# Kernel tuning notes

Measured on AMD Instinct MI355X. Metric: run time of the kernel, lower is better.

The kernel has to match this reference:

```python
import jax, jax.numpy as jnp
import numpy as np

RADIUS = 0.1
WEIGHT = 0.2
MATMUL_NORM = False


def setup_inputs() -> dict:
    key = jax.random.key(0)
    k1, k2, k3, k4, k5 = jax.random.split(key, 5)
    S, B, Ck, Cv, H, W = 8, 2, 64, 64, 64, 64
    return {
        "memory_keys": jax.random.normal(k1, (S, B, Ck, H, W), jnp.float32),
        "memory_values": jax.random.normal(k2, (S, B, Cv, H, W), jnp.float32),
        "query_query": jax.random.normal(k3, (B, Ck, H, W), jnp.float32),
        "disparity": jax.random.normal(k4, (B, 1, H, W), jnp.float32),
        "sequence_index": jax.random.randint(k5, (B, S, 2), 0, 10, jnp.int32),
    }


def reference(memory_keys, memory_values, query_query, disparity, sequence_index):
    S, B, Ck, H, W = memory_keys.shape
    Cv = memory_values.shape[2]
    HW, SHW = H * W, S * H * W

    # keys: [B, Ck, S*H*W]; queries: [B, H*W, Ck]
    keys = jnp.transpose(memory_keys, (1, 2, 0, 3, 4)).reshape(B, Ck, SHW)
    q = jnp.transpose(query_query.reshape(B, Ck, HW), (0, 2, 1))

    # disparity-based additive mask, vectorized over frames
    weight = WEIGHT / S / H / W
    idx = sequence_index.astype(jnp.float32)
    dist = jnp.sqrt((idx[:, :, 1] - 5.0) ** 2 + (idx[:, :, 0] - 5.0) ** 2)  # [B, S]
    total_disp = dist[:, :, None, None] * disparity  # [B, S, H, W] (disparity [B,1,H,W])
    mask = jnp.where(jnp.abs(total_disp) > RADIUS, weight, 0.0).reshape(B, 1, SHW)

    attn = jnp.einsum("bnc,bcm->bnm", q, keys)  # [B, HW, SHW]
    if MATMUL_NORM:
        attn = attn * (Ck ** -0.5)
    attn = jax.nn.softmax(attn, axis=-1) + mask

    vals = jnp.transpose(memory_values, (1, 0, 3, 4, 2)).reshape(B, SHW, Cv)
    out = jnp.einsum("bnm,bmv->bnv", attn, vals)  # [B, HW, Cv]
    return jnp.transpose(out, (0, 2, 1)).reshape(B, Cv, H, W)
```

## Files before the change

### kernel.cpp

```cpp
#include <hip/hip_runtime.h>
#include <hip/hip_bf16.h>
#include <stdint.h>

#define NS   8
#define NB   2
#define CK   64
#define CV   64
#define HWN  4096
#define SHW  32768
#define RADIUS_ 0.1f
#define MASK_W  6.103515625e-6f

#define TM    32
#define NW    8
#define QS_STR 68
#define P_STR  40
#define SBIAS 24.0f
#define LOG2E 1.4426950408889634f
#define SBIAS2 34.624680981135326f
#define KS    4

#define KT_ELEMS (NS * NB * CK * HWN)
#define KT_BYTES ((size_t)KT_ELEMS * 2)
#define VB_BYTES ((size_t)KT_ELEMS * 2)
#define MASKP_OFF (KT_BYTES + VB_BYTES)
#define WS_NEED  (MASKP_OFF + 4096)
#define ONUM_OFF (MASKP_OFF + 4096)
#define ONUM_BYTES ((size_t)KS * NB * HWN * CV * 4)
#define ODEN_OFF (ONUM_OFF + ONUM_BYTES)
#define ODEN_BYTES ((size_t)KS * NB * HWN * 4)
#define WS2      (ODEN_OFF + ODEN_BYTES)

typedef __bf16    bf16x8 __attribute__((ext_vector_type(8)));
typedef _Float16  f16x8  __attribute__((ext_vector_type(8)));
typedef float     f32x4  __attribute__((ext_vector_type(4)));
typedef unsigned short u16x8 __attribute__((ext_vector_type(8)));
typedef uint32_t  u32x2 __attribute__((ext_vector_type(2)));
typedef uint32_t  u32x4 __attribute__((ext_vector_type(4)));

__device__ __forceinline__ unsigned short f2bfu(float x) {
  __hip_bfloat16 h = __float2bfloat16(x);
  return __builtin_bit_cast(unsigned short, h);
}
__device__ __forceinline__ bf16x8 ld_bf8_lds(const unsigned short* p) {
  u16x8 u = *(const u16x8*)p;
  return __builtin_bit_cast(bf16x8, u);
}
__device__ __forceinline__ void load_lds16(const void* g, void* l) {
  __builtin_amdgcn_global_load_lds(
      (const __attribute__((address_space(1))) unsigned int*)g,
      (__attribute__((address_space(3))) unsigned int*)l, 16, 0, 0);
}


__global__ __launch_bounds__(512) void prep_all(
    const float* __restrict__ keys, const float* __restrict__ vals,
    const float* __restrict__ disp, const int* __restrict__ seq,
    _Float16* __restrict__ kT, unsigned short* __restrict__ vbf,
    float* __restrict__ maskpart)
{
  const int t = threadIdx.x;
  const int blk = blockIdx.x;
  if (blk < 512) {
    __shared__ _Float16 lds[128 * 64];
    const int chunk = blk & 31;
    const int s     = (blk >> 5) & 7;
    const int b     = blk >> 8;
    const int hw0   = chunk * 128;
    const int c_st  = t >> 3;
    const int msub  = (t & 7) * 8;
    const int cchunk = c_st >> 3;
    const int clow   = c_st & 7;

    const float* krow = keys + ((size_t)((s * NB + b) * CK + c_st)) * HWN + hw0;
    #pragma unroll
    for (int r = 0; r < 2; ++r) {
      const int m0 = msub + r * 64;
      f32x4 k0 = *(const f32x4*)(krow + m0);
      f32x4 k1 = *(const f32x4*)(krow + m0 + 4);
      const int swz = (cchunk ^ ((m0 >> 3) & 7)) * 8 + clow;
      #pragma unroll
      for (int j = 0; j < 4; ++j) {
        lds[(m0 + j)     * 64 + swz] = (_Float16)k0[j];
        lds[(m0 + 4 + j) * 64 + swz] = (_Float16)k1[j];
      }
    }
    __syncthreads();

    _Float16* kout = kT + ((size_t)(b * SHW + s * HWN + hw0)) * CK;
    const int mm = t >> 3;
    const int cg = t & 7;
    #pragma unroll
    for (int r2 = 0; r2 < 2; ++r2) {
      const int m   = mm + r2 * 64;
      const int swz = cg ^ ((m >> 3) & 7);
      u16x8 v = *(const u16x8*)&lds[m * 64 + swz * 8];
      *(u16x8*)(kout + (size_t)m * CK + cg * 8) = v;
    }
  } else {
    const int r = blk - 512;
    const int s = r >> 7;
    const int b = (r >> 6) & 1;
    const int c = r & 63;
    float j0 = (float)seq[(b * NS + s) * 2 + 0];
    float j1 = (float)seq[(b * NS + s) * 2 + 1];
    const float dist = sqrtf((j1 - 5.f) * (j1 - 5.f) + (j0 - 5.f) * (j0 - 5.f));

    const size_t i = (size_t)r * HWN + t * 8;
    const int hw = t * 8;
    f32x4 a  = *(const f32x4*)(vals + i);
    f32x4 bb = *(const f32x4*)(vals + i + 4);
    f32x4 d0 = *(const f32x4*)(disp + (size_t)b * HWN + hw);
    f32x4 d1 = *(const f32x4*)(disp + (size_t)b * HWN + hw + 4);
    u16x8 o;
    float acc = 0.f;
    #pragma unroll
    for (int j = 0; j < 4; ++j) {
      o[j]     = f2bfu(a[j]);
      o[4 + j] = f2bfu(bb[j]);
      if (fabsf(dist * d0[j]) > RADIUS_) acc += a[j];
      if (fabsf(dist * d1[j]) > RADIUS_) acc += bb[j];
    }
    {
      const int m  = t & 3;
      const int pa = ((2 * m) & 3) * 2 + (m >> 1);
      const int pb = ((2 * m + 1) & 3) * 2 + (m >> 1);
      unsigned short* rowp = vbf + (size_t)r * HWN + (t >> 2) * 32;
      u32x4 wv = __builtin_bit_cast(u32x4, o);
      *(u32x2*)(rowp + pa * 4) = (u32x2){wv.x, wv.y};
      *(u32x2*)(rowp + pb * 4) = (u32x2){wv.z, wv.w};
    }

    #pragma unroll
    for (int m2 = 32; m2 >= 1; m2 >>= 1) acc += __shfl_xor(acc, m2);
    __shared__ float red[8];
    if ((t & 63) == 0) red[t >> 6] = acc;
    __syncthreads();
    if (t == 0) {
      float s8 = 0.f;
      #pragma unroll
      for (int j = 0; j < 8; ++j) s8 += red[j];
      maskpart[(b * CV + c) * NS + s] = MASK_W * s8;
    }
  }
}

struct __align__(16) Smem6 {
  union {
    struct {
      _Float16       kbuf[2][128 * 64];
      unsigned short vbuf[2][64 * 128];
    } main;
    struct {
      float obuf[4][32][64];
      float dbuf[4][32];
    } epi;
    float qs[64 * QS_STR];
  };
};

__global__ __launch_bounds__(512, 4) void attn_v6(
    const _Float16* __restrict__ kT,
    const unsigned short* __restrict__ vbf,
    const float* __restrict__ query,
    float* __restrict__ onum,
    float* __restrict__ odenom)
{
  __shared__ Smem6 sm;
  const int t    = threadIdx.x;
  const int w    = t >> 6;
  const int lane = t & 63;
  const int quad = lane >> 4;
  const int l15  = lane & 15;
  const int kq   = w & 3;
  const int rg   = w >> 2;
  const int bidx = blockIdx.x;
  const int xcd  = bidx & 7;
  const int b    = xcd & 1;
  const int ks   = xcd >> 1;
  const int tile = bidx >> 3;
  const int n0   = tile * 64;

  {
    const int qc   = t >> 3;
    const int noff = (t & 7) * 8;
    const int slot = qc ^ ((t & 7) << 2);
    const float* qp = query + (size_t)(b * CK + qc) * HWN + n0 + noff;
    f32x4 q0 = *(const f32x4*)(qp);
    f32x4 q1 = *(const f32x4*)(qp + 4);
    #pragma unroll
    for (int j = 0; j < 4; ++j) {
      sm.qs[(noff + j)     * QS_STR + slot] = q0[j];
      sm.qs[(noff + 4 + j) * QS_STR + slot] = q1[j];
    }
  }
  __syncthreads();
  f16x8 qf[2][2];
  #pragma unroll
  for (int f = 0; f < 2; ++f) {
    const int n  = rg * 32 + f * 16 + l15;
    const int sw = ((n >> 3) & 7) << 2;
    const float* base = &sm.qs[n * QS_STR];
    #pragma unroll
    for (int h = 0; h < 2; ++h) {
      const int c0 = (h * 32 + quad * 8) ^ sw;
      f32x4 a  = *(const f32x4*)(base + c0);
      f32x4 bb = *(const f32x4*)(base + (c0 ^ 4));
      f16x8 q;
      #pragma unroll
      for (int j = 0; j < 4; ++j) {
        q[j]     = (_Float16)(a[j]  * LOG2E);
        q[4 + j] = (_Float16)(bb[j] * LOG2E);
      }
      qf[f][h] = q;
    }
  }
  __syncthreads();

  f32x4 Of[2][4];
  f32x4 Ol[2];
  #pragma unroll
  for (int f = 0; f < 2; ++f) {
    #pragma unroll
    for (int cf = 0; cf < 4; ++cf) Of[f][cf] = (f32x4){0.f, 0.f, 0.f, 0.f};
    Ol[f] = (f32x4){0.f, 0.f, 0.f, 0.f};
  }
  bf16x8 vones;
  #pragma unroll
  for (int i = 0; i < 8; ++i)
    vones[i] = __builtin_bit_cast(__bf16, (unsigned short)0x3F80);

  uint32_t ksrc_off[2];
  int      kldsoff[2];
  uint32_t vsrc_off[2];
  int      vldsoff[2];
  #pragma unroll
  for (int j = 0; j < 2; ++j) {
    const int inst = w * 2 + j;
    const int kl   = inst * 8 + (lane >> 3);
    const int cqs  = lane & 7;
    ksrc_off[j] = (uint32_t)(kl * 128 + ((cqs ^ (kl & 7)) * 16));
    kldsoff[j]  = inst * 1024;
    const int cv  = inst * 4 + (lane >> 4);
    const int chs = (lane & 15) ^ (cv & 7);
    vsrc_off[j] = (uint32_t)(cv * HWN + chs * 8);
    vldsoff[j]  = inst * 1024;
  }
  const char* kgbase = (const char*)(kT + (size_t)b * SHW * CK);
  const int   kbase0 = ks * (SHW / KS);

  {
    const char* kg = kgbase + (size_t)kbase0 * 128;
    load_lds16(kg + ksrc_off[0], (char*)sm.main.kbuf[0] + kldsoff[0]);
    load_lds16(kg + ksrc_off[1], (char*)sm.main.kbuf[0] + kldsoff[1]);
    const int sfrm0 = kbase0 >> 12;
    const unsigned short* vg =
        vbf + (size_t)((sfrm0 * NB + b) * CV) * HWN + (kbase0 & 4095);
    load_lds16(vg + vsrc_off[0], (char*)sm.main.vbuf[0] + vldsoff[0]);
    load_lds16(vg + vsrc_off[1], (char*)sm.main.vbuf[0] + vldsoff[1]);
  }

  for (int it = 0; it < 64; ++it) {
    const int cur  = it & 1;
    const int key0 = kbase0 + it * 128;

    __syncthreads();

    if (it < 63) {
      const int keyn = key0 + 128;
      const char* kg = kgbase + (size_t)keyn * 128;
      load_lds16(kg + ksrc_off[0], (char*)sm.main.kbuf[cur ^ 1] + kldsoff[0]);
      load_lds16(kg + ksrc_off[1], (char*)sm.main.kbuf[cur ^ 1] + kldsoff[1]);
      const int sfrmn = keyn >> 12;
      const unsigned short* vg =
          vbf + (size_t)((sfrmn * NB + b) * CV) * HWN + (keyn & 4095);
      load_lds16(vg + vsrc_off[0], (char*)sm.main.vbuf[cur ^ 1] + vldsoff[0]);
      load_lds16(vg + vsrc_off[1], (char*)sm.main.vbuf[cur ^ 1] + vldsoff[1]);
    }

    f16x8 kf[2][2];
    #pragma unroll
    for (int g = 0; g < 2; ++g) {
      const int kl  = kq * 32 + g * 16 + l15;
      const int swz = kl & 7;
      const _Float16* kb = &sm.main.kbuf[cur][kl * 64];
      #pragma unroll
      for (int h = 0; h < 2; ++h) {
        const int slot = (h * 4 + quad) ^ swz;
        kf[g][h] = *(const f16x8*)(kb + slot * 8);
      }
    }

    bf16x8 vf[4];
    {
      const int ch = kq * 4 + quad;
      #pragma unroll
      for (int cf = 0; cf < 4; ++cf) {
        const int cv  = cf * 16 + l15;
        const int swz = cv & 7;
        vf[cf] = ld_bf8_lds(&sm.main.vbuf[cur][cv * 128 + ((ch ^ swz) << 3)]);
      }
    }

    f32x4 sf[2][2];
    #pragma unroll
    for (int g = 0; g < 2; ++g)
      #pragma unroll
      for (int f = 0; f < 2; ++f) {
        f32x4 acc = (f32x4){-SBIAS2, -SBIAS2, -SBIAS2, -SBIAS2};
        acc = __builtin_amdgcn_mfma_f32_16x16x32_f16(kf[g][0], qf[f][0], acc, 0, 0, 0);
        acc = __builtin_amdgcn_mfma_f32_16x16x32_f16(kf[g][1], qf[f][1], acc, 0, 0, 0);
        sf[g][f] = acc;
      }

    #pragma unroll
    for (int f = 0; f < 2; ++f) {
      uint32_t pk[2][2];
      #pragma unroll
      for (int g = 0; g < 2; ++g) {
        float e0 = __builtin_amdgcn_exp2f(sf[g][f][0]);
        float e1 = __builtin_amdgcn_exp2f(sf[g][f][1]);
        float e2 = __builtin_amdgcn_exp2f(sf[g][f][2]);
        float e3 = __builtin_amdgcn_exp2f(sf[g][f][3]);
        pk[g][0] = __builtin_amdgcn_perm(__builtin_bit_cast(uint32_t, e1),
                                         __builtin_bit_cast(uint32_t, e0),
                                         0x07060302u);
        pk[g][1] = __builtin_amdgcn_perm(__builtin_bit_cast(uint32_t, e3),
                                         __builtin_bit_cast(uint32_t, e2),
                                         0x07060302u);
      }
      bf16x8 pf = __builtin_bit_cast(bf16x8,
          (u32x4){pk[0][0], pk[0][1], pk[1][0], pk[1][1]});

      #pragma unroll
      for (int cf = 0; cf < 4; ++cf)
        Of[f][cf] = __builtin_amdgcn_mfma_f32_16x16x32_bf16(pf, vf[cf], Of[f][cf], 0, 0, 0);
      Ol[f] = __builtin_amdgcn_mfma_f32_16x16x32_bf16(pf, vones, Ol[f], 0, 0, 0);
    }
  }

  __syncthreads();

  #pragma unroll
  for (int phase = 0; phase < 2; ++phase) {
    if (rg == phase) {
      #pragma unroll
      for (int f = 0; f < 2; ++f)
        #pragma unroll
        for (int r = 0; r < 4; ++r) {
          const int row = f * 16 + quad * 4 + r;
          if (l15 == 0) sm.epi.dbuf[kq][row] = Ol[f][r];
          #pragma unroll
          for (int cf = 0; cf < 4; ++cf)
            sm.epi.obuf[kq][row][cf * 16 + l15] = Of[f][cf][r];
        }
    }
    __syncthreads();
    {
      const int row = t >> 4;
      const int v4  = (t & 15) * 4;
      f32x4 acc = *(const f32x4*)&sm.epi.obuf[0][row][v4];
      #pragma unroll
      for (int q = 1; q < 4; ++q)
        acc += *(const f32x4*)&sm.epi.obuf[q][row][v4];
      *(f32x4*)&onum[((size_t)(ks * NB + b) * HWN + n0 + phase * 32 + row) * CV + v4] = acc;
      if (t < 32) {
        float d = sm.epi.dbuf[0][t] + sm.epi.dbuf[1][t] +
                  sm.epi.dbuf[2][t] + sm.epi.dbuf[3][t];
        odenom[(size_t)(ks * NB + b) * HWN + n0 + phase * 32 + t] = d;
      }
    }
    __syncthreads();
  }
}

__global__ __launch_bounds__(256) void finalize_k(
    const float* __restrict__ onum, const float* __restrict__ odenom,
    const float* __restrict__ maskpart, float* __restrict__ out)
{
  __shared__ float tile[64][68];
  __shared__ float dinv[64];
  __shared__ float ml[64];
  const int t   = threadIdx.x;
  const int b   = blockIdx.x >> 6;
  const int hw0 = (blockIdx.x & 63) * 64;

  #pragma unroll
  for (int pass = 0; pass < 4; ++pass) {
    const int row = pass * 16 + (t >> 4);
    const int v4  = (t & 15) * 4;
    f32x4 acc = (f32x4){0.f, 0.f, 0.f, 0.f};
    #pragma unroll
    for (int ks = 0; ks < KS; ++ks)
      acc += *(const f32x4*)&onum[((size_t)(ks * NB + b) * HWN + hw0 + row) * CV + v4];
    *(f32x4*)&tile[row][v4] = acc;
  }
  if (t < 64) {
    float d = 0.f;
    #pragma unroll
    for (int ks = 0; ks < KS; ++ks)
      d += odenom[(size_t)(ks * NB + b) * HWN + hw0 + t];
    dinv[t] = 1.f / fmaxf(d, 1e-30f);
  }
  if (t >= 64 && t < 128) {
    float m = 0.f;
    #pragma unroll
    for (int s = 0; s < NS; ++s) m += maskpart[(b * CV + (t - 64)) * NS + s];
    ml[t - 64] = m;
  }
  __syncthreads();

  #pragma unroll
  for (int pass = 0; pass < 4; ++pass) {
    const int v   = pass * 16 + (t >> 4);
    const int hw4 = (t & 15) * 4;
    f32x4 o;
    #pragma unroll
    for (int j = 0; j < 4; ++j)
      o[j] = tile[hw4 + j][v] * dinv[hw4 + j] + ml[v];
    *(f32x4*)&out[((size_t)(b * CV + v)) * HWN + hw0 + hw4] = o;
  }
}

struct __align__(16) SmemF {
  union {
    float qs[TM * QS_STR];
    unsigned short p[NW][2][16 * P_STR];
    struct {
      float obuf[NW][TM][CV];
      float lbuf[NW][TM];
    } epi;
  };
};

__global__ __launch_bounds__(512) void attn_fast(
    const _Float16* __restrict__ kT, const unsigned short* __restrict__ vbf,
    const float* __restrict__ query, const float* __restrict__ maskpart,
    float* __restrict__ out)
{
  __shared__ SmemF sm;
  const int t    = threadIdx.x;
  const int w    = t >> 6;
  const int lane = t & 63;
  const int quad = lane >> 4;
  const int l15  = lane & 15;
  const int bidx = blockIdx.x;
  const int b    = bidx & 1;
  const int n0   = ((bidx >> 1) & 127) * TM;

  if (t < 256) {
    const int qc   = t >> 2;
    const int noff = (t & 3) * 8;
    const int slot = qc ^ ((t & 3) << 2);
    const float* qp = query + (size_t)(b * CK + qc) * HWN + n0 + noff;
    f32x4 q0 = *(const f32x4*)(qp);
    f32x4 q1 = *(const f32x4*)(qp + 4);
    #pragma unroll
    for (int j = 0; j < 4; ++j) {
      sm.qs[(noff + j)     * QS_STR + slot] = q0[j];
      sm.qs[(noff + 4 + j) * QS_STR + slot] = q1[j];
    }
  }
  __syncthreads();
  f16x8 qf[2][2];
  #pragma unroll
  for (int f = 0; f < 2; ++f) {
    const int n  = f * 16 + l15;
    const int sw = ((n >> 3) & 7) << 2;
    const float* base = &sm.qs[n * QS_STR];
    #pragma unroll
    for (int h = 0; h < 2; ++h) {
      const int c0 = (h * 32 + quad * 8) ^ sw;
      f32x4 a  = *(const f32x4*)(base + c0);
      f32x4 bb = *(const f32x4*)(base + (c0 ^ 4));
      f16x8 q;
      #pragma unroll
      for (int j = 0; j < 4; ++j) { q[j] = (_Float16)a[j]; q[4 + j] = (_Float16)bb[j]; }
      qf[f][h] = q;
    }
  }
  __syncthreads();

  f32x4 Of[2][4];
  f32x4 Ol[2];
  #pragma unroll
  for (int f = 0; f < 2; ++f) {
    #pragma unroll
    for (int cf = 0; cf < 4; ++cf) Of[f][cf] = (f32x4){0.f, 0.f, 0.f, 0.f};
    Ol[f] = (f32x4){0.f, 0.f, 0.f, 0.f};
  }
  bf16x8 vones;
  #pragma unroll
  for (int i = 0; i < 8; ++i)
    vones[i] = __builtin_bit_cast(__bf16, (unsigned short)0x3F80);

  const _Float16* kbase = kT + (size_t)b * SHW * CK;

  for (int it = 0; it < SHW / 256; ++it) {
    const int key0 = it * 256 + w * 32;
    f16x8 kf[2][2];
    #pragma unroll
    for (int g = 0; g < 2; ++g)
      #pragma unroll
      for (int h = 0; h < 2; ++h)
        kf[g][h] = *(const f16x8*)(kbase +
            (size_t)(key0 + g * 16 + l15) * CK + h * 32 + quad * 8);

    const int s   = it >> 4;
    const int hwg = (it & 15) * 256 + w * 32;
    const int pa  = ((2 * quad) & 3) * 2 + (quad >> 1);
    const int pb  = ((2 * quad + 1) & 3) * 2 + (quad >> 1);
    bf16x8 vf[4];
    #pragma unroll
    for (int cf = 0; cf < 4; ++cf) {
      const unsigned short* rowp = vbf +
          ((size_t)((s * NB + b) * CV + cf * 16 + l15)) * HWN + hwg;
      u32x2 lo = *(const u32x2*)(rowp + pa * 4);
      u32x2 hi = *(const u32x2*)(rowp + pb * 4);
      vf[cf] = __builtin_bit_cast(bf16x8, (u32x4){lo.x, lo.y, hi.x, hi.y});
    }

    f32x4 sfv[2][2];
    #pragma unroll
    for (int f = 0; f < 2; ++f)
      #pragma unroll
      for (int g = 0; g < 2; ++g) {
        f32x4 acc = (f32x4){0.f, 0.f, 0.f, 0.f};
        acc = __builtin_amdgcn_mfma_f32_16x16x32_f16(qf[f][0], kf[g][0], acc, 0, 0, 0);
        acc = __builtin_amdgcn_mfma_f32_16x16x32_f16(qf[f][1], kf[g][1], acc, 0, 0, 0);
        sfv[f][g] = acc;
      }

    #pragma unroll
    for (int f = 0; f < 2; ++f)
      #pragma unroll
      for (int g = 0; g < 2; ++g)
        #pragma unroll
        for (int r = 0; r < 4; ++r)
          sfv[f][g][r] = __expf(sfv[f][g][r] - SBIAS);

    #pragma unroll
    for (int f = 0; f < 2; ++f)
      #pragma unroll
      for (int g = 0; g < 2; ++g)
        #pragma unroll
        for (int r = 0; r < 4; ++r)
          sm.p[w][f][(quad * 4 + r) * P_STR + g * 16 + l15] = f2bfu(sfv[f][g][r]);
    asm volatile("s_waitcnt lgkmcnt(0)" ::: "memory");
    bf16x8 pf[2];
    #pragma unroll
    for (int f = 0; f < 2; ++f)
      pf[f] = ld_bf8_lds(&sm.p[w][f][l15 * P_STR + quad * 8]);

    #pragma unroll
    for (int f = 0; f < 2; ++f) {
      #pragma unroll
      for (int cf = 0; cf < 4; ++cf)
        Of[f][cf] = __builtin_amdgcn_mfma_f32_16x16x32_bf16(pf[f], vf[cf], Of[f][cf], 0, 0, 0);
      Ol[f] = __builtin_amdgcn_mfma_f32_16x16x32_bf16(pf[f], vones, Ol[f], 0, 0, 0);
    }
  }

  __syncthreads();
  #pragma unroll
  for (int f = 0; f < 2; ++f)
    #pragma unroll
    for (int r = 0; r < 4; ++r) {
      const int row = f * 16 + quad * 4 + r;
      if (l15 == 0) sm.epi.lbuf[w][row] = Ol[f][r];
      #pragma unroll
      for (int cf = 0; cf < 4; ++cf)
        sm.epi.obuf[w][row][cf * 16 + l15] = Of[f][cf][r];
    }
  __syncthreads();
  {
    const int n   = t & 31;
    const int vhi = t >> 5;
    float denom = 0.f;
    #pragma unroll
    for (int ww = 0; ww < NW; ++ww) denom += sm.epi.lbuf[ww][n];
    const float inv = 1.f / fmaxf(denom, 1e-30f);
    #pragma unroll
    for (int g = 0; g < 4; ++g) {
      const int v = vhi + 16 * g;
      float num = 0.f;
      #pragma unroll
      for (int ww = 0; ww < NW; ++ww) num += sm.epi.obuf[ww][n][v];
      float mlv = 0.f;
      #pragma unroll
      for (int s = 0; s < NS; ++s) mlv += maskpart[(b * CV + v) * NS + s];
      out[((size_t)(b * CV + v)) * HWN + n0 + n] = num * inv + mlv;
    }
  }
}

extern "C" void kernel_launch(void* const* d_in, const int* in_sizes, int n_in,
                              void* d_out, int out_size, void* d_ws, size_t ws_size,
                              hipStream_t stream) {
  const float* keys  = (const float*)d_in[0];
  const float* vals  = (const float*)d_in[1];
  const float* query = (const float*)d_in[2];
  const float* disp  = (const float*)d_in[3];
  const int*   seq   = (const int*)d_in[4];
  float*       out   = (float*)d_out;

  _Float16*       kT    = (_Float16*)d_ws;
  unsigned short* vbf   = (unsigned short*)((char*)d_ws + KT_BYTES);
  float*          maskp = (float*)((char*)d_ws + MASKP_OFF);

  prep_all<<<512 + NB * NS * CV, 512, 0, stream>>>(keys, vals, disp, seq,
                                                   kT, vbf, maskp);

  if (ws_size >= WS2) {
    float* onum   = (float*)((char*)d_ws + ONUM_OFF);
    float* odenom = (float*)((char*)d_ws + ODEN_OFF);
    attn_v6<<<NB * 64 * KS, 512, 0, stream>>>(kT, vbf, query, onum, odenom);
    finalize_k<<<NB * (HWN / 64), 256, 0, stream>>>(onum, odenom, maskp, out);
  } else {
    attn_fast<<<NB * (HWN / TM), 512, 0, stream>>>(kT, vbf, query, maskp, out);
  }
}
```

Baseline: 161.4 us.

## Double query tile per block to 128 with 1024 threads and prioritize MFMA

Each attention block now covers 128 queries with 16 waves instead of 64 queries with 8 waves. Every K/V tile staged in LDS is therefore reused by twice as many queries, and each thread issues one async load per tile instead of two. The grid is halved and the epilogue reduction runs in four phases. s_setprio is raised around the MFMA sections to favour matrix issue over other waves. The risk is register pressure under the 1024-thread launch bound and fewer blocks to hide latency with.

```diff
diff --git a/kernel.cpp b/kernel.cpp
--- a/kernel.cpp
+++ b/kernel.cpp
@@ -155,11 +155,11 @@
       float obuf[4][32][64];
       float dbuf[4][32];
     } epi;
-    float qs[64 * QS_STR];
+    float qs[128 * QS_STR];
   };
 };
 
-__global__ __launch_bounds__(512, 4) void attn_v6(
+__global__ __launch_bounds__(1024, 4) void attn_v6(
     const _Float16* __restrict__ kT,
     const unsigned short* __restrict__ vbf,
     const float* __restrict__ query,
@@ -179,12 +179,12 @@
   const int b    = xcd & 1;
   const int ks   = xcd >> 1;
   const int tile = bidx >> 3;
-  const int n0   = tile * 64;
+  const int n0   = tile * 128;
 
   {
-    const int qc   = t >> 3;
-    const int noff = (t & 7) * 8;
-    const int slot = qc ^ ((t & 7) << 2);
+    const int qc   = t >> 4;
+    const int noff = (t & 15) * 8;
+    const int slot = qc ^ ((t & 15) << 2);
     const float* qp = query + (size_t)(b * CK + qc) * HWN + n0 + noff;
     f32x4 q0 = *(const f32x4*)(qp);
     f32x4 q1 = *(const f32x4*)(qp + 4);
@@ -199,7 +199,7 @@
   #pragma unroll
   for (int f = 0; f < 2; ++f) {
     const int n  = rg * 32 + f * 16 + l15;
-    const int sw = ((n >> 3) & 7) << 2;
+    const int sw = ((n >> 3) & 15) << 2;
     const float* base = &sm.qs[n * QS_STR];
     #pragma unroll
     for (int h = 0; h < 2; ++h) {
@@ -230,34 +230,24 @@
   for (int i = 0; i < 8; ++i)
     vones[i] = __builtin_bit_cast(__bf16, (unsigned short)0x3F80);
 
-  uint32_t ksrc_off[2];
-  int      kldsoff[2];
-  uint32_t vsrc_off[2];
-  int      vldsoff[2];
-  #pragma unroll
-  for (int j = 0; j < 2; ++j) {
-    const int inst = w * 2 + j;
-    const int kl   = inst * 8 + (lane >> 3);
-    const int cqs  = lane & 7;
-    ksrc_off[j] = (uint32_t)(kl * 128 + ((cqs ^ (kl & 7)) * 16));
-    kldsoff[j]  = inst * 1024;
-    const int cv  = inst * 4 + (lane >> 4);
-    const int chs = (lane & 15) ^ (cv & 7);
-    vsrc_off[j] = (uint32_t)(cv * HWN + chs * 8);
-    vldsoff[j]  = inst * 1024;
-  }
+  const int kl   = w * 8 + (lane >> 3);
+  const uint32_t ksrc_off = (uint32_t)(kl * 128 + (((lane & 7) ^ (kl & 7)) * 16));
+  const int kldsoff = w * 1024;
+  const int cvr  = w * 4 + (lane >> 4);
+  const uint32_t vsrc_off =
+      (uint32_t)(cvr * HWN + (((lane & 15) ^ (cvr & 7)) * 8));
+  const int vldsoff = w * 1024;
+
   const char* kgbase = (const char*)(kT + (size_t)b * SHW * CK);
   const int   kbase0 = ks * (SHW / KS);
 
   {
     const char* kg = kgbase + (size_t)kbase0 * 128;
-    load_lds16(kg + ksrc_off[0], (char*)sm.main.kbuf[0] + kldsoff[0]);
-    load_lds16(kg + ksrc_off[1], (char*)sm.main.kbuf[0] + kldsoff[1]);
+    load_lds16(kg + ksrc_off, (char*)sm.main.kbuf[0] + kldsoff);
     const int sfrm0 = kbase0 >> 12;
     const unsigned short* vg =
         vbf + (size_t)((sfrm0 * NB + b) * CV) * HWN + (kbase0 & 4095);
-    load_lds16(vg + vsrc_off[0], (char*)sm.main.vbuf[0] + vldsoff[0]);
-    load_lds16(vg + vsrc_off[1], (char*)sm.main.vbuf[0] + vldsoff[1]);
+    load_lds16(vg + vsrc_off, (char*)sm.main.vbuf[0] + vldsoff);
   }
 
   for (int it = 0; it < 64; ++it) {
@@ -269,21 +259,19 @@
     if (it < 63) {
       const int keyn = key0 + 128;
       const char* kg = kgbase + (size_t)keyn * 128;
-      load_lds16(kg + ksrc_off[0], (char*)sm.main.kbuf[cur ^ 1] + kldsoff[0]);
-      load_lds16(kg + ksrc_off[1], (char*)sm.main.kbuf[cur ^ 1] + kldsoff[1]);
+      load_lds16(kg + ksrc_off, (char*)sm.main.kbuf[cur ^ 1] + kldsoff);
       const int sfrmn = keyn >> 12;
       const unsigned short* vg =
           vbf + (size_t)((sfrmn * NB + b) * CV) * HWN + (keyn & 4095);
-      load_lds16(vg + vsrc_off[0], (char*)sm.main.vbuf[cur ^ 1] + vldsoff[0]);
-      load_lds16(vg + vsrc_off[1], (char*)sm.main.vbuf[cur ^ 1] + vldsoff[1]);
+      load_lds16(vg + vsrc_off, (char*)sm.main.vbuf[cur ^ 1] + vldsoff);
     }
 
     f16x8 kf[2][2];
     #pragma unroll
     for (int g = 0; g < 2; ++g) {
-      const int kl  = kq * 32 + g * 16 + l15;
-      const int swz = kl & 7;
-      const _Float16* kb = &sm.main.kbuf[cur][kl * 64];
+      const int klr = kq * 32 + g * 16 + l15;
+      const int swz = klr & 7;
+      const _Float16* kb = &sm.main.kbuf[cur][klr * 64];
       #pragma unroll
       for (int h = 0; h < 2; ++h) {
         const int slot = (h * 4 + quad) ^ swz;
@@ -303,6 +291,7 @@
     }
 
     f32x4 sf[2][2];
+    __builtin_amdgcn_s_setprio(1);
     #pragma unroll
     for (int g = 0; g < 2; ++g)
       #pragma unroll
@@ -312,6 +301,7 @@
         acc = __builtin_amdgcn_mfma_f32_16x16x32_f16(kf[g][1], qf[f][1], acc, 0, 0, 0);
         sf[g][f] = acc;
       }
+    __builtin_amdgcn_s_setprio(0);
 
     #pragma unroll
     for (int f = 0; f < 2; ++f) {
@@ -332,17 +322,19 @@
       bf16x8 pf = __builtin_bit_cast(bf16x8,
           (u32x4){pk[0][0], pk[0][1], pk[1][0], pk[1][1]});
 
+      __builtin_amdgcn_s_setprio(1);
       #pragma unroll
       for (int cf = 0; cf < 4; ++cf)
         Of[f][cf] = __builtin_amdgcn_mfma_f32_16x16x32_bf16(pf, vf[cf], Of[f][cf], 0, 0, 0);
       Ol[f] = __builtin_amdgcn_mfma_f32_16x16x32_bf16(pf, vones, Ol[f], 0, 0, 0);
-    }
-  }
-
-  __syncthreads();
-
-  #pragma unroll
-  for (int phase = 0; phase < 2; ++phase) {
+      __builtin_amdgcn_s_setprio(0);
+    }
+  }
+
+  __syncthreads();
+
+  #pragma unroll
+  for (int phase = 0; phase < 4; ++phase) {
     if (rg == phase) {
       #pragma unroll
       for (int f = 0; f < 2; ++f)
@@ -356,7 +348,7 @@
         }
     }
     __syncthreads();
-    {
+    if (t < 512) {
       const int row = t >> 4;
       const int v4  = (t & 15) * 4;
       f32x4 acc = *(const f32x4*)&sm.epi.obuf[0][row][v4];
@@ -614,7 +606,7 @@
   if (ws_size >= WS2) {
     float* onum   = (float*)((char*)d_ws + ONUM_OFF);
     float* odenom = (float*)((char*)d_ws + ODEN_OFF);
-    attn_v6<<<NB * 64 * KS, 512, 0, stream>>>(kT, vbf, query, onum, odenom);
+    attn_v6<<<NB * 32 * KS, 1024, 0, stream>>>(kT, vbf, query, onum, odenom);
     finalize_k<<<NB * (HWN / 64), 256, 0, stream>>>(onum, odenom, maskp, out);
   } else {
     attn_fast<<<NB * (HWN / TM), 512, 0, stream>>>(kT, vbf, query, maskp, out);
```

After: 157.5 us. 1.02x faster.
